# Kernel optimization log

Measured on AMD Instinct MI355X. Metric: run time of the kernel, lower is better.

Reference implementation:

```python
import jax, jax.numpy as jnp
import numpy as np

# dims (match init_kwargs)
S = 2048      # sequence_length
H = 2048      # hidden_size
NH = 32       # num_attention_heads
KVH = 8       # num_key_value_heads
HD = 64       # head_dim
WIN = 128     # sliding_window
QM = NH // KVH
SM_SCALE = 1.0 / float(np.sqrt(HD))


def _rope_rotate(x, cos, sin):
    # x: [S, n, HD]; cos/sin: [S, HD//2]
    x1, x2 = jnp.split(x, 2, axis=-1)
    c = cos[:, None, :].astype(x.dtype)
    s = sin[:, None, :].astype(x.dtype)
    return jnp.concatenate([x1 * c - x2 * s, x2 * c + x1 * s], axis=-1)


def setup_inputs() -> dict:
    key = jax.random.key(0)
    ks = jax.random.split(key, 6)
    x = jax.random.normal(ks[0], (S, H), jnp.float32)
    qkv_dim = HD * (NH + 2 * KVH)
    qkv_kernel = jax.random.normal(ks[1], (H, qkv_dim), jnp.float32) * 0.02
    qkv_bias = jnp.zeros((qkv_dim,), jnp.float32)
    out_kernel = jax.random.normal(ks[2], (NH * HD, H), jnp.float32) * 0.02
    out_bias = jnp.zeros((H,), jnp.float32)
    sinks = jax.random.normal(ks[3], (NH,), jnp.float32) * 0.02
    # RoPE tables: [S, HD//2]
    pos = np.arange(S, dtype=np.float32)
    inv_freq = 1.0 / (10000.0 ** (np.arange(HD // 2, dtype=np.float32) / (HD // 2)))
    ang = pos[:, None] * inv_freq[None, :]
    cos_table = jnp.asarray(np.cos(ang), jnp.float32)
    sin_table = jnp.asarray(np.sin(ang), jnp.float32)
    # causal + sliding-window additive mask [S, S]
    qi = np.arange(S, dtype=np.int32)[:, None]
    ki = np.arange(S, dtype=np.int32)[None, :]
    m = np.where(ki > qi, -np.inf, 0.0).astype(np.float32)
    m = np.where(ki < qi - WIN, -np.inf, m).astype(np.float32)
    mask = jnp.asarray(m)
    return {"x": x, "qkv_kernel": qkv_kernel, "qkv_bias": qkv_bias,
            "out_kernel": out_kernel, "out_bias": out_bias, "sinks": sinks,
            "cos_table": cos_table, "sin_table": sin_table, "mask": mask}


def reference(x, qkv_kernel, qkv_bias, out_kernel, out_bias, sinks, cos_table, sin_table, mask):
    xf = x.astype(jnp.float32)
    qkv = jnp.dot(xf, qkv_kernel, precision=jax.lax.Precision.HIGHEST) + qkv_bias  # [S, qkv_dim]
    q_end = NH * HD
    k_end = q_end + KVH * HD
    q = qkv[:, :q_end].reshape(S, NH, HD)          # NH = KVH*QM
    k = qkv[:, q_end:k_end].reshape(S, KVH, HD)
    v = qkv[:, k_end:].reshape(S, KVH, HD)
    q = _rope_rotate(q, cos_table, sin_table).reshape(S, KVH, QM, HD)
    k = _rope_rotate(k, cos_table, sin_table)
    # logits: [KVH, QM, S_q, S_k]; K broadcast across q_mult (GQA)
    logits = jnp.einsum('qhmd,khd->hmqk', q, k) * jnp.float32(SM_SCALE)
    logits = logits + mask[None, None, :, :]
    sink = jnp.broadcast_to(sinks.reshape(KVH, QM, 1, 1).astype(jnp.float32), (KVH, QM, S, 1))
    extended = jnp.concatenate([logits, sink], axis=-1)
    weights = jax.nn.softmax(extended, axis=-1)[..., :-1]
    attn = jnp.einsum('hmqk,khd->qhmd', weights, v).reshape(S, NH * HD)
    out = jnp.dot(attn, out_kernel, precision=jax.lax.Precision.HIGHEST) + out_bias
    return out.astype(x.dtype)
```

## Files before the change

### kernel.cpp

```cpp
#include <hip/hip_runtime.h>
#include <hip/hip_bf16.h>
#include <cstdint>

typedef __hip_bfloat16 bf16;
typedef __attribute__((ext_vector_type(8))) __bf16 bf16x8;
typedef __attribute__((ext_vector_type(4))) float f32x4;

static __device__ __forceinline__ void gload_lds16(const void* g, void* l) {
  __builtin_amdgcn_global_load_lds(
      (const __attribute__((address_space(1))) uint32_t*)g,
      (__attribute__((address_space(3))) uint32_t*)l, 16, 0, 0);
}

__global__ __launch_bounds__(256)
void prep_kernel(const float* __restrict__ x, const float* __restrict__ w1,
                 const float* __restrict__ w2, bf16* __restrict__ xb,
                 bf16* __restrict__ w1t, bf16* __restrict__ w2t) {
  __shared__ float tile[32][33];
  const int lin = blockIdx.x;
  const int t = threadIdx.x;
  if (lin < 4096) {
    const int i = lin * 256 + t;
    const float4 v = reinterpret_cast<const float4*>(x)[i];
    ushort4 o;
    o.x = __builtin_bit_cast(unsigned short, __float2bfloat16(v.x));
    o.y = __builtin_bit_cast(unsigned short, __float2bfloat16(v.y));
    o.z = __builtin_bit_cast(unsigned short, __float2bfloat16(v.z));
    o.w = __builtin_bit_cast(unsigned short, __float2bfloat16(v.w));
    reinterpret_cast<ushort4*>(xb)[i] = o;
    return;
  }
  const float* in;
  bf16* out;
  int R, C, bx, by;
  if (lin < 10240) {
    const int tl = lin - 4096;
    in = w1; out = w1t; R = 2048; C = 3072; bx = tl % 96; by = tl / 96;
  } else {
    const int tl = lin - 10240;
    in = w2; out = w2t; R = 2048; C = 2048; bx = tl & 63; by = tl >> 6;
  }
  const int c0 = bx * 32, r0 = by * 32;
  const int tx = t & 31, ty = t >> 5;
#pragma unroll
  for (int i = 0; i < 4; ++i)
    tile[ty + i * 8][tx] = in[(size_t)(r0 + ty + i * 8) * C + c0 + tx];
  __syncthreads();
#pragma unroll
  for (int i = 0; i < 4; ++i)
    out[(size_t)(c0 + ty + i * 8) * R + r0 + tx] = __float2bfloat16(tile[tx][ty + i * 8]);
}

template <int NH, int SSHIFT>
__global__ void rope_kernel(bf16* __restrict__ buf, const float* __restrict__ cosT,
                            const float* __restrict__ sinT) {
  const int idx = blockIdx.x * 256 + threadIdx.x;
  const int c = idx & 3;
  const int h = (idx >> 2) & (NH - 1);
  const int s = idx >> SSHIFT;
  bf16* p = buf + (size_t)s * (NH * 64) + h * 64 + c * 8;
  bf16x8 v1 = *reinterpret_cast<bf16x8*>(p);
  bf16x8 v2 = *reinterpret_cast<bf16x8*>(p + 32);
  const float4 c0 = *reinterpret_cast<const float4*>(&cosT[s * 32 + c * 8]);
  const float4 c1 = *reinterpret_cast<const float4*>(&cosT[s * 32 + c * 8 + 4]);
  const float4 s0 = *reinterpret_cast<const float4*>(&sinT[s * 32 + c * 8]);
  const float4 s1 = *reinterpret_cast<const float4*>(&sinT[s * 32 + c * 8 + 4]);
  const float cs[8] = {c0.x, c0.y, c0.z, c0.w, c1.x, c1.y, c1.z, c1.w};
  const float sn[8] = {s0.x, s0.y, s0.z, s0.w, s1.x, s1.y, s1.z, s1.w};
  bf16x8 o1, o2;
#pragma unroll
  for (int e = 0; e < 8; ++e) {
    const float x1 = (float)v1[e], x2 = (float)v2[e];
    o1[e] = (__bf16)(x1 * cs[e] - x2 * sn[e]);
    o2[e] = (__bf16)(x2 * cs[e] + x1 * sn[e]);
  }
  *reinterpret_cast<bf16x8*>(p) = o1;
  *reinterpret_cast<bf16x8*>(p + 32) = o2;
}

__global__ __launch_bounds__(512, 1)
void gemm1_kernel(const bf16* __restrict__ A, const bf16* __restrict__ Bt,
                  const float* __restrict__ bias,
                  bf16* __restrict__ qb, bf16* __restrict__ kb, bf16* __restrict__ vt) {
  extern __shared__ __align__(16) char smem[];
  constexpr int K = 2048, NK = 32;
  const int lin = blockIdx.x;
  const int wgid = (lin & 7) * 32 + (lin >> 3);
  const int bx = wgid >> 4, by = wgid & 15;
  const int brow = by * 128, bcol = bx * 192;
  const int t = threadIdx.x, lane = t & 63, w = t >> 6;
  const int wr = w >> 2, wc = w & 3;
  const int rr = lane & 15, rg = lane >> 4;

  char* Ab = smem;
  char* Bb = smem + 49152;

  auto stageA = [&](int kt) {
#pragma unroll
    for (int p = 0; p < 2; ++p) {
      const int idx = p * 512 + t;
      const int row = idx >> 3;
      const int cg = (idx & 7) ^ (row & 7);
      gload_lds16(A + (size_t)(brow + row) * K + kt * 64 + cg * 8,
                  Ab + (size_t)(kt % 3) * 16384 + (p * 512 + (t & ~63)) * 16);
    }
  };
  auto stageB = [&](int kt) {
#pragma unroll
    for (int p = 0; p < 3; ++p) {
      const int idx = p * 512 + t;
      const int row = idx >> 3;
      const int cg = (idx & 7) ^ (row & 7);
      gload_lds16(Bt + (size_t)(bcol + row) * K + kt * 64 + cg * 8,
                  Bb + (size_t)(kt % 3) * 24576 + (p * 512 + (t & ~63)) * 16);
    }
  };

  f32x4 acc[4][3];
#pragma unroll
  for (int i = 0; i < 4; ++i)
#pragma unroll
    for (int j = 0; j < 3; ++j) acc[i][j] = f32x4{0.f, 0.f, 0.f, 0.f};

  stageA(0); stageB(0); stageA(1); stageB(1);
  asm volatile("s_waitcnt vmcnt(5)" ::: "memory");
  __builtin_amdgcn_s_barrier();

  for (int kt = 0; kt < NK; ++kt) {
    const char* Ar = Ab + (size_t)(kt % 3) * 16384;
    const char* Br = Bb + (size_t)(kt % 3) * 24576;
#pragma unroll
    for (int ks = 0; ks < 2; ++ks) {
      bf16x8 af[4], bfr[3];
      const int c = ks * 4 + rg;
#pragma unroll
      for (int i = 0; i < 4; ++i) {
        const int row = wr * 64 + i * 16 + rr;
        af[i] = *reinterpret_cast<const bf16x8*>(Ar + row * 128 + ((c ^ (row & 7)) * 16));
      }
#pragma unroll
      for (int j = 0; j < 3; ++j) {
        const int row = wc * 48 + j * 16 + rr;
        bfr[j] = *reinterpret_cast<const bf16x8*>(Br + row * 128 + ((c ^ (row & 7)) * 16));
      }
      if (kt + 2 < NK) {
        if (ks == 0) stageA(kt + 2);
        else         stageB(kt + 2);
      }
      asm volatile("s_waitcnt lgkmcnt(0)" ::: "memory");
      __builtin_amdgcn_sched_barrier(0);
      __builtin_amdgcn_s_setprio(1);
#pragma unroll
      for (int i = 0; i < 4; ++i)
#pragma unroll
        for (int j = 0; j < 3; ++j)
          acc[i][j] = __builtin_amdgcn_mfma_f32_16x16x32_bf16(af[i], bfr[j], acc[i][j], 0, 0, 0);
      __builtin_amdgcn_s_setprio(0);
    }
    if (kt + 2 < NK)      asm volatile("s_waitcnt vmcnt(5)" ::: "memory");
    else if (kt + 1 < NK) asm volatile("s_waitcnt vmcnt(0)" ::: "memory");
    if (kt + 1 < NK) __builtin_amdgcn_s_barrier();
  }

#pragma unroll
  for (int j = 0; j < 3; ++j) {
    const int gcf = bcol + wc * 48 + j * 16;
    const int gc = gcf + rr;
    const float bv = bias[gc];
    if (gcf < 2048) {
#pragma unroll
      for (int i = 0; i < 4; ++i) {
        const int s0 = brow + wr * 64 + i * 16 + rg * 4;
#pragma unroll
        for (int r = 0; r < 4; ++r)
          qb[(size_t)(s0 + r) * 2048 + gc] = __float2bfloat16(acc[i][j][r] + bv);
      }
    } else if (gcf < 2560) {
      const int kc = gc - 2048;
#pragma unroll
      for (int i = 0; i < 4; ++i) {
        const int s0 = brow + wr * 64 + i * 16 + rg * 4;
#pragma unroll
        for (int r = 0; r < 4; ++r)
          kb[(size_t)(s0 + r) * 512 + kc] = __float2bfloat16(acc[i][j][r] + bv);
      }
    } else {
      const int vcol = gc - 2560;
#pragma unroll
      for (int i = 0; i < 4; ++i) {
        ushort4 o;
        o.x = __builtin_bit_cast(unsigned short, __float2bfloat16(acc[i][j][0] + bv));
        o.y = __builtin_bit_cast(unsigned short, __float2bfloat16(acc[i][j][1] + bv));
        o.z = __builtin_bit_cast(unsigned short, __float2bfloat16(acc[i][j][2] + bv));
        o.w = __builtin_bit_cast(unsigned short, __float2bfloat16(acc[i][j][3] + bv));
        *reinterpret_cast<ushort4*>(
            &vt[(size_t)vcol * 2048 + brow + wr * 64 + i * 16 + rg * 4]) = o;
      }
    }
  }
}

__global__ __launch_bounds__(512, 1)
void gemm2_kernel(const bf16* __restrict__ A, const bf16* __restrict__ Bt,
                  const float* __restrict__ bias, float* __restrict__ C) {
  extern __shared__ __align__(16) char smem[];
  constexpr int K = 2048, NK = 32;
  const int lin = blockIdx.x;
  const int wgid = (lin & 7) * 32 + (lin >> 3);
  const int bx = wgid >> 4, by = wgid & 15;
  const int brow = by * 128, bcol = bx * 128;
  const int t = threadIdx.x, lane = t & 63, w = t >> 6;
  const int wr = w & 3, wc = w >> 2;
  const int rr = lane & 15, rg = lane >> 4;

  char* Ab = smem;
  char* Bb = smem + 49152;

  auto stage = [&](int kt) {
#pragma unroll
    for (int p = 0; p < 2; ++p) {
      const int idx = p * 512 + t;
      const int row = idx >> 3;
      const int cg = (idx & 7) ^ (row & 7);
      gload_lds16(A + (size_t)(brow + row) * K + kt * 64 + cg * 8,
                  Ab + (size_t)(kt % 3) * 16384 + (p * 512 + (t & ~63)) * 16);
      gload_lds16(Bt + (size_t)(bcol + row) * K + kt * 64 + cg * 8,
                  Bb + (size_t)(kt % 3) * 16384 + (p * 512 + (t & ~63)) * 16);
    }
  };

  f32x4 acc[2][4];
#pragma unroll
  for (int i = 0; i < 2; ++i)
#pragma unroll
    for (int j = 0; j < 4; ++j) acc[i][j] = f32x4{0.f, 0.f, 0.f, 0.f};

  stage(0); stage(1);
  asm volatile("s_waitcnt vmcnt(4)" ::: "memory");
  __builtin_amdgcn_s_barrier();

  for (int kt = 0; kt < NK; ++kt) {
    const char* Ar = Ab + (size_t)(kt % 3) * 16384;
    const char* Br = Bb + (size_t)(kt % 3) * 16384;
#pragma unroll
    for (int ks = 0; ks < 2; ++ks) {
      bf16x8 af[2], bfr[4];
      const int c = ks * 4 + rg;
#pragma unroll
      for (int i = 0; i < 2; ++i) {
        const int row = wr * 32 + i * 16 + rr;
        af[i] = *reinterpret_cast<const bf16x8*>(Ar + row * 128 + ((c ^ (row & 7)) * 16));
      }
#pragma unroll
      for (int j = 0; j < 4; ++j) {
        const int row = wc * 64 + j * 16 + rr;
        bfr[j] = *reinterpret_cast<const bf16x8*>(Br + row * 128 + ((c ^ (row & 7)) * 16));
      }
      if (kt + 2 < NK && ks == 0) stage(kt + 2);
      asm volatile("s_waitcnt lgkmcnt(0)" ::: "memory");
      __builtin_amdgcn_sched_barrier(0);
      __builtin_amdgcn_s_setprio(1);
#pragma unroll
      for (int i = 0; i < 2; ++i)
#pragma unroll
        for (int j = 0; j < 4; ++j)
          acc[i][j] = __builtin_amdgcn_mfma_f32_16x16x32_bf16(af[i], bfr[j], acc[i][j], 0, 0, 0);
      __builtin_amdgcn_s_setprio(0);
    }
    if (kt + 2 < NK)      asm volatile("s_waitcnt vmcnt(4)" ::: "memory");
    else if (kt + 1 < NK) asm volatile("s_waitcnt vmcnt(0)" ::: "memory");
    if (kt + 1 < NK) __builtin_amdgcn_s_barrier();
  }

#pragma unroll
  for (int i = 0; i < 2; ++i)
#pragma unroll
    for (int j = 0; j < 4; ++j) {
      const int gc = bcol + wc * 64 + j * 16 + rr;
      const float bv = bias[gc];
      const int r0 = brow + wr * 32 + i * 16 + rg * 4;
#pragma unroll
      for (int r = 0; r < 4; ++r)
        C[(size_t)(r0 + r) * 2048 + gc] = acc[i][j][r] + bv;
    }
}

__global__ __launch_bounds__(256, 2)
void attn_kernel(const bf16* __restrict__ Q, const bf16* __restrict__ Kb,
                 const bf16* __restrict__ Vt, const float* __restrict__ sinks,
                 const float* __restrict__ cosT, const float* __restrict__ sinT,
                 bf16* __restrict__ aout) {
  extern __shared__ __align__(16) char smem[];
  const int hk = blockIdx.x;
  const int q0 = blockIdx.y * 32;
  const int k0 = q0 - 128;
  const int t = threadIdx.x, w = t >> 6, lane = t & 63;
  const int cl = lane & 15, rg = lane >> 4;
  const int head = hk * 4 + w;

  char* Ks = smem;
  char* Ps = smem + 20480 + w * 12288;

#pragma unroll
  for (int p = 0; p < 5; ++p) {
    const int idx = p * 256 + t;
    const int row = idx >> 3, c = idx & 7;
    int key = k0 + row;
    if (key < 0) key = 0;
    gload_lds16(Kb + (size_t)key * 512 + hk * 64 + ((c ^ (row & 7)) << 3),
                Ks + (size_t)(p * 256 + (t & ~63)) * 16);
  }

  bf16x8 aq[2][2];
#pragma unroll
  for (int qf = 0; qf < 2; ++qf) {
    const int qrow = q0 + qf * 16 + cl;
    const bf16* qp = Q + (size_t)qrow * 2048 + head * 64 + rg * 8;
    const bf16x8 q1 = *reinterpret_cast<const bf16x8*>(qp);
    const bf16x8 q2 = *reinterpret_cast<const bf16x8*>(qp + 32);
    const float4 c0 = *reinterpret_cast<const float4*>(&cosT[qrow * 32 + rg * 8]);
    const float4 c1 = *reinterpret_cast<const float4*>(&cosT[qrow * 32 + rg * 8 + 4]);
    const float4 s0 = *reinterpret_cast<const float4*>(&sinT[qrow * 32 + rg * 8]);
    const float4 s1 = *reinterpret_cast<const float4*>(&sinT[qrow * 32 + rg * 8 + 4]);
    const float cs[8] = {c0.x, c0.y, c0.z, c0.w, c1.x, c1.y, c1.z, c1.w};
    const float sn[8] = {s0.x, s0.y, s0.z, s0.w, s1.x, s1.y, s1.z, s1.w};
#pragma unroll
    for (int e = 0; e < 8; ++e) {
      const float x1 = (float)q1[e], x2 = (float)q2[e];
      aq[qf][0][e] = (__bf16)(x1 * cs[e] - x2 * sn[e]);
      aq[qf][1][e] = (__bf16)(x2 * cs[e] + x1 * sn[e]);
    }
  }
  __syncthreads();

  f32x4 acc[2][10];
#pragma unroll
  for (int qf = 0; qf < 2; ++qf)
#pragma unroll
    for (int nf = 0; nf < 10; ++nf) acc[qf][nf] = f32x4{0.f, 0.f, 0.f, 0.f};

#pragma unroll
  for (int nf = 0; nf < 10; ++nf) {
    const int row = nf * 16 + cl;
    bf16x8 bk[2];
#pragma unroll
    for (int ks = 0; ks < 2; ++ks) {
      const int chunk = ks * 4 + rg;
      bk[ks] = *reinterpret_cast<const bf16x8*>(
          Ks + row * 128 + ((chunk ^ (row & 7)) << 4));
    }
#pragma unroll
    for (int qf = 0; qf < 2; ++qf)
#pragma unroll
      for (int ks = 0; ks < 2; ++ks)
        acc[qf][nf] = __builtin_amdgcn_mfma_f32_16x16x32_bf16(aq[qf][ks], bk[ks], acc[qf][nf], 0, 0, 0);
  }

  bf16x8 vb[5][4];
#pragma unroll
  for (int ks = 0; ks < 5; ++ks) {
    int key = k0 + ks * 32 + rg * 8;
    if (key < 0) key = 0;
#pragma unroll
    for (int j = 0; j < 4; ++j)
      vb[ks][j] = *reinterpret_cast<const bf16x8*>(
          Vt + ((size_t)hk * 64 + j * 16 + cl) * 2048 + key);
  }

  const float sinkv = sinks[head];
  const float scale = 0.125f;
  const int cfloor = 128 - q0;
#pragma unroll
  for (int qf = 0; qf < 2; ++qf)
#pragma unroll
    for (int r = 0; r < 4; ++r) {
      const int rowb = qf * 16 + rg * 4 + r;
      int cmin = rowb;
      if (cfloor > cmin) cmin = cfloor;
      const int cmax = rowb + 128;
      float m = sinkv;
      float pv[10];
#pragma unroll
      for (int nf = 0; nf < 10; ++nf) {
        const int cc = nf * 16 + cl;
        float lv = (cc >= cmin && cc <= cmax) ? acc[qf][nf][r] * scale : -INFINITY;
        pv[nf] = lv;
        m = fmaxf(m, lv);
      }
#pragma unroll
      for (int off = 1; off < 16; off <<= 1)
        m = fmaxf(m, __shfl_xor(m, off, 64));
      float sum = 0.f;
#pragma unroll
      for (int nf = 0; nf < 10; ++nf) {
        const float p = __expf(pv[nf] - m);
        pv[nf] = p;
        sum += p;
      }
#pragma unroll
      for (int off = 1; off < 16; off <<= 1)
        sum += __shfl_xor(sum, off, 64);
      sum += __expf(sinkv - m);
      const float inv = 1.f / sum;
#pragma unroll
      for (int nf = 0; nf < 10; ++nf) {
        const int col = nf * 16 + cl;
        const int chunk = col >> 3;
        *reinterpret_cast<bf16*>(Ps + rowb * 384 + ((chunk ^ (rowb & 7)) << 4) + (cl & 7) * 2) =
            __float2bfloat16(pv[nf] * inv);
      }
    }

  asm volatile("s_waitcnt lgkmcnt(0)" ::: "memory");
  __builtin_amdgcn_sched_barrier(0);

  f32x4 oacc[2][4];
#pragma unroll
  for (int qf = 0; qf < 2; ++qf)
#pragma unroll
    for (int j = 0; j < 4; ++j) oacc[qf][j] = f32x4{0.f, 0.f, 0.f, 0.f};

#pragma unroll
  for (int ks = 0; ks < 5; ++ks) {
    bf16x8 pa[2];
#pragma unroll
    for (int qf = 0; qf < 2; ++qf) {
      const int row = qf * 16 + cl;
      const int chunk = ks * 4 + rg;
      pa[qf] = *reinterpret_cast<const bf16x8*>(
          Ps + row * 384 + ((chunk ^ (row & 7)) << 4));
    }
#pragma unroll
    for (int j = 0; j < 4; ++j)
#pragma unroll
      for (int qf = 0; qf < 2; ++qf)
        oacc[qf][j] = __builtin_amdgcn_mfma_f32_16x16x32_bf16(pa[qf], vb[ks][j], oacc[qf][j], 0, 0, 0);
  }

#pragma unroll
  for (int qf = 0; qf < 2; ++qf)
#pragma unroll
    for (int j = 0; j < 4; ++j)
#pragma unroll
      for (int r = 0; r < 4; ++r) {
        const int gr = q0 + qf * 16 + rg * 4 + r;
        const int gc = head * 64 + j * 16 + cl;
        aout[(size_t)gr * 2048 + gc] = __float2bfloat16(oacc[qf][j][r]);
      }
}

extern "C" void kernel_launch(void* const* d_in, const int* in_sizes, int n_in,
                              void* d_out, int out_size, void* d_ws, size_t ws_size,
                              hipStream_t stream) {
  const float* x     = (const float*)d_in[0];
  const float* w1    = (const float*)d_in[1];
  const float* b1    = (const float*)d_in[2];
  const float* w2    = (const float*)d_in[3];
  const float* b2    = (const float*)d_in[4];
  const float* sinks = (const float*)d_in[5];
  const float* cosT  = (const float*)d_in[6];
  const float* sinT  = (const float*)d_in[7];
  float* out = (float*)d_out;

  char* ws = (char*)d_ws;
  bf16* xb   = (bf16*)(ws);
  bf16* w1t  = (bf16*)(ws + 8388608);
  bf16* w2t  = (bf16*)(ws + 20971520);
  bf16* qbuf = (bf16*)(ws + 29360128);
  bf16* kbuf = (bf16*)(ws + 37748736);
  bf16* vt   = (bf16*)(ws + 39845888);
  bf16* attn = (bf16*)(ws + 41943040);
  (void)in_sizes; (void)n_in; (void)out_size; (void)ws_size;

  prep_kernel<<<14336, 256, 0, stream>>>(x, w1, w2, xb, w1t, w2t);
  gemm1_kernel<<<256, 512, 122880, stream>>>(xb, w1t, b1, qbuf, kbuf, vt);
  rope_kernel<8, 5><<<256, 256, 0, stream>>>(kbuf, cosT, sinT);
  attn_kernel<<<dim3(8, 64), 256, 69632, stream>>>(qbuf, kbuf, vt, sinks, cosT, sinT, attn);
  gemm2_kernel<<<256, 512, 98304, stream>>>(attn, w2t, b2, out);
}
```

Measured before the change: 86.85 us.

## Stage V tile through LDS via async loads and coalesce attention output stores

The attention kernel now reuses the K staging region to bring the transposed V tile into LDS with global_load_lds, using a rotated slot swizzle, instead of having each wave load V fragments from global memory into registers. The output is also staged through the per-wave P buffers in LDS and written back as 16-byte coalesced rows, replacing scattered 2-byte bf16 stores. This cuts redundant global V traffic across the four waves and makes writes coalesced, at the cost of extra __syncthreads barriers and serialising V loading after QK^T.

```diff
diff --git a/kernel.cpp b/kernel.cpp
--- a/kernel.cpp
+++ b/kernel.cpp
@@ -299,6 +299,7 @@
   const int head = hk * 4 + w;
 
   char* Ks = smem;
+  char* Vs = smem;
   char* Ps = smem + 20480 + w * 12288;
 
 #pragma unroll
@@ -356,15 +357,22 @@
         acc[qf][nf] = __builtin_amdgcn_mfma_f32_16x16x32_bf16(aq[qf][ks], bk[ks], acc[qf][nf], 0, 0, 0);
   }
 
-  bf16x8 vb[5][4];
-#pragma unroll
-  for (int ks = 0; ks < 5; ++ks) {
-    int key = k0 + ks * 32 + rg * 8;
-    if (key < 0) key = 0;
-#pragma unroll
-    for (int j = 0; j < 4; ++j)
-      vb[ks][j] = *reinterpret_cast<const bf16x8*>(
-          Vt + ((size_t)hk * 64 + j * 16 + cl) * 2048 + key);
+  __syncthreads();
+
+  {
+    const bf16* vbase = Vt + (size_t)hk * 64 * 2048;
+#pragma unroll
+    for (int p = 0; p < 5; ++p) {
+      const int idx = p * 256 + t;
+      const int row = idx / 20;
+      const int slot = idx - row * 20;
+      int src = slot - (row & 7);
+      if (src < 0) src += 20;
+      int key = k0 + src * 8;
+      if (key < 0) key = 0;
+      gload_lds16(vbase + (size_t)row * 2048 + key,
+                  Vs + (size_t)(p * 256 + (t & ~63)) * 16);
+    }
   }
 
   const float sinkv = sinks[head];
@@ -411,8 +419,9 @@
       }
     }
 
-  asm volatile("s_waitcnt lgkmcnt(0)" ::: "memory");
+  asm volatile("s_waitcnt vmcnt(0) lgkmcnt(0)" ::: "memory");
   __builtin_amdgcn_sched_barrier(0);
+  __syncthreads();
 
   f32x4 oacc[2][4];
 #pragma unroll
@@ -431,22 +440,40 @@
           Ps + row * 384 + ((chunk ^ (row & 7)) << 4));
     }
 #pragma unroll
+    for (int j = 0; j < 4; ++j) {
+      const int d = j * 16 + cl;
+      int slot = ks * 4 + rg + (d & 7);
+      if (slot >= 20) slot -= 20;
+      const bf16x8 bv = *reinterpret_cast<const bf16x8*>(Vs + d * 320 + slot * 16);
+#pragma unroll
+      for (int qf = 0; qf < 2; ++qf)
+        oacc[qf][j] = __builtin_amdgcn_mfma_f32_16x16x32_bf16(pa[qf], bv, oacc[qf][j], 0, 0, 0);
+    }
+  }
+
+#pragma unroll
+  for (int qf = 0; qf < 2; ++qf)
+#pragma unroll
     for (int j = 0; j < 4; ++j)
 #pragma unroll
-      for (int qf = 0; qf < 2; ++qf)
-        oacc[qf][j] = __builtin_amdgcn_mfma_f32_16x16x32_bf16(pa[qf], vb[ks][j], oacc[qf][j], 0, 0, 0);
-  }
-
-#pragma unroll
-  for (int qf = 0; qf < 2; ++qf)
-#pragma unroll
-    for (int j = 0; j < 4; ++j)
-#pragma unroll
       for (int r = 0; r < 4; ++r) {
-        const int gr = q0 + qf * 16 + rg * 4 + r;
-        const int gc = head * 64 + j * 16 + cl;
-        aout[(size_t)gr * 2048 + gc] = __float2bfloat16(oacc[qf][j][r]);
-      }
+        const int row = qf * 16 + rg * 4 + r;
+        const int colb = (j * 16 + cl) * 2;
+        *reinterpret_cast<bf16*>(Ps + row * 384 + (colb ^ ((row & 7) << 4))) =
+            __float2bfloat16(oacc[qf][j][r]);
+      }
+  __syncthreads();
+
+#pragma unroll
+  for (int p = 0; p < 4; ++p) {
+    const int idx = p * 256 + t;
+    const int row = idx >> 5;
+    const int j16 = idx & 31;
+    const int w2 = j16 >> 3, c8 = j16 & 7;
+    const uint4 v = *reinterpret_cast<const uint4*>(
+        smem + 20480 + w2 * 12288 + row * 384 + ((c8 * 16) ^ ((row & 7) << 4)));
+    *reinterpret_cast<uint4*>(aout + (size_t)(q0 + row) * 2048 + hk * 256 + j16 * 8) = v;
+  }
 }
 
 extern "C" void kernel_launch(void* const* d_in, const int* in_sizes, int n_in,
```

Result: no change. 85.79 us (-1.2%).
